# Kernel tuning notes

Measured on AMD Instinct MI355X. Metric: run time of the kernel, lower is better.

## Reference

```python
import jax, jax.numpy as jnp
import numpy as np
from itertools import permutations

M = 10          # number of masked tokens (logits.size(0) when whole_word=False)
VOCAB = 50257   # n_class


def setup_inputs() -> dict:
    key = jax.random.key(0)
    k1, k2 = jax.random.split(key)
    logits = jax.random.normal(k1, (M, VOCAB), dtype=jnp.float32)
    target = jax.random.randint(k2, (M,), 0, VOCAB, dtype=jnp.int64).astype(jnp.int32)
    # All M! permutations, enumerated exactly as itertools.permutations (lexicographic),
    # matching the torch module's iteration order (ties broken by first strict improvement).
    perms = jnp.asarray(np.array(list(permutations(range(M))), dtype=np.int32))
    return {"logits": logits, "target": target, "perms": perms}


def reference(logits, target, perms):
    # prob[i, v] = softmax over classes
    prob = jax.nn.softmax(logits, axis=-1)                      # [M, V]
    # S[i, j] = prob[i, target[j]]  (score of assigning slot j's target to position i)
    S = prob[:, target]                                         # [M, M]
    # score(p) = sum_i prob[i, target[p[i]]] = sum_i S[i, p[i]]
    rows = jnp.arange(S.shape[0], dtype=jnp.int32)[None, :]     # [1, M]
    scores = S[rows, perms].sum(axis=-1)                        # [P]
    # torch loop keeps the FIRST permutation achieving the max (strict > update);
    # jnp.argmax also returns the first occurrence of the max.
    best = jnp.argmax(scores)
    target_best = target[perms[best]]                           # [M]
    # CrossEntropyLoss(reduction='none') == -log_softmax gathered at target
    logp = jax.nn.log_softmax(logits, axis=-1)                  # [M, V]
    loss = -jnp.take_along_axis(logp, target_best[:, None].astype(jnp.int32), axis=1)[:, 0]
    return loss, target_best
```

## Files before the change

kernel.cpp:

```cpp
#include <hip/hip_runtime.h>

#define VOCAB 50257
#define M 10
#define NPERM 3628800
#define CHUNKS 16
#define CH 3144
#define NTHREADS_PERM 30240
#define PERM_BLOCKS 119

#define WS_PSUM 0

__global__ __launch_bounds__(256) void chunkstats_kernel(
    const float* __restrict__ logits, float* __restrict__ ws) {
    const int r = blockIdx.x >> 4;
    const int c = blockIdx.x & 15;
    const size_t rowoff = (size_t)r * VOCAB;
    const float* __restrict__ x = logits + rowoff;
    const int s = c * CH;
    const int e = (s + CH < VOCAB) ? s + CH : VOCAB;
    const int tid = threadIdx.x;
    const int j0 = s + (int)((4u - ((unsigned)rowoff & 3u)) & 3u);
    const int j1 = j0 + ((e - j0) & ~3);
    __shared__ float wred[4];

    float sum = 0.f;
    for (int j = s + tid; j < j0; j += 256) sum += __expf(x[j]);
    for (int j = j0 + 4 * tid; j < j1; j += 1024) {
        const float4 v = *(const float4*)(x + j);
        sum += expf(v.x) + expf(v.y) + expf(v.z) + expf(v.w);
    }
    for (int j = j1 + tid; j < e; j += 256) sum += expf(x[j]);
    #pragma unroll
    for (int off = 32; off; off >>= 1) sum += __shfl_down(sum, off, 64);
    if ((tid & 63) == 0) wred[tid >> 6] = sum;
    __syncthreads();
    if (tid == 0)
        ws[WS_PSUM + blockIdx.x] = wred[0] + wred[1] + wred[2] + wred[3];
}

__global__ __launch_bounds__(256) void perm_kernel(
    const float* __restrict__ logits, const int* __restrict__ target,
    const float* __restrict__ ws, unsigned long long* __restrict__ keys) {
    __shared__ float S[100], rowsum[10];
    __shared__ unsigned long long wk[4];
    const int tid = threadIdx.x;

    if (tid < 160) {
        float c = ws[WS_PSUM + tid];
        #pragma unroll
        for (int off = 8; off; off >>= 1) c += __shfl_xor(c, off, 16);
        if ((tid & 15) == 0) rowsum[tid >> 4] = c;
    }
    __syncthreads();
    if (tid < 100) {
        const int i = tid / 10, k = tid % 10;
        S[tid] = expf(logits[(size_t)i * VOCAB + target[k]]) / rowsum[i];
    }
    __syncthreads();

    const unsigned int t = blockIdx.x * 256u + tid;
    unsigned long long key = 0ull;
    if (t < NTHREADS_PERM) {
        const unsigned int base = t * 120u;
        unsigned int p = base;
        unsigned long long avail = 0x9876543210ull;
        float prefix = 0.f;
        const unsigned int fact5[5] = {362880u, 40320u, 5040u, 720u, 120u};
        #pragma unroll
        for (int pos = 0; pos < 5; ++pos) {
            const unsigned int f = fact5[pos];
            const unsigned int d = p / f;
            p -= d * f;
            const unsigned int sh = d * 4u;
            const unsigned int sym = (unsigned int)(avail >> sh) & 0xFu;
            avail = (avail & ((1ull << sh) - 1ull)) | ((avail >> (sh + 4u)) << sh);
            prefix += S[pos * 10 + sym];
        }
        float s5v[5], s6v[5], s7v[5], s8v[5], s9v[5];
        #pragma unroll
        for (int j = 0; j < 5; ++j) {
            const int q = (int)((avail >> (4 * j)) & 0xFull);
            s5v[j] = S[50 + q]; s6v[j] = S[60 + q]; s7v[j] = S[70 + q];
            s8v[j] = S[80 + q]; s9v[j] = S[90 + q];
        }
        float best = -1.f; unsigned int bl = 0; unsigned int l = 0;
        #pragma unroll
        for (int a = 0; a < 5; ++a) {
            const float pa = prefix + s5v[a];
            #pragma unroll
            for (int b = 0; b < 5; ++b) {
                if (b == a) continue;
                const float pb = pa + s6v[b];
                #pragma unroll
                for (int c = 0; c < 5; ++c) {
                    if (c == a || c == b) continue;
                    const float pc = pb + s7v[c];
                    #pragma unroll
                    for (int d = 0; d < 5; ++d) {
                        if (d == a || d == b || d == c) continue;
                        const int e = 10 - a - b - c - d;
                        const float sc = (pc + s8v[d]) + s9v[e];
                        if (sc > best) { best = sc; bl = l; }
                        ++l;
                    }
                }
            }
        }
        const unsigned int gidx = base + bl;
        key = ((unsigned long long)__float_as_uint(best) << 32) |
              (unsigned long long)(0xFFFFFFFFu - gidx);
    }
    #pragma unroll
    for (int off = 32; off; off >>= 1) {
        const unsigned long long o = __shfl_down(key, off, 64);
        if (o > key) key = o;
    }
    if ((tid & 63) == 0) wk[tid >> 6] = key;
    __syncthreads();
    if (tid == 0) {
        unsigned long long k = wk[0];
        #pragma unroll
        for (int w = 1; w < 4; ++w) if (wk[w] > k) k = wk[w];
        keys[blockIdx.x] = k;
    }
}

__global__ __launch_bounds__(256) void final_kernel(
    const float* __restrict__ logits, const int* __restrict__ target,
    const float* __restrict__ ws, const unsigned long long* __restrict__ keys,
    float* __restrict__ out) {
    __shared__ float rowsum[10];
    __shared__ unsigned long long wk[4];
    __shared__ int perm[10];
    const int tid = threadIdx.x;

    if (tid < 160) {
        float c = ws[WS_PSUM + tid];
        #pragma unroll
        for (int off = 8; off; off >>= 1) c += __shfl_xor(c, off, 16);
        if ((tid & 15) == 0) rowsum[tid >> 4] = c;
    }

    unsigned long long k = (tid < PERM_BLOCKS) ? keys[tid] : 0ull;
    #pragma unroll
    for (int off = 32; off; off >>= 1) {
        const unsigned long long o = __shfl_down(k, off, 64);
        if (o > k) k = o;
    }
    if ((tid & 63) == 0) wk[tid >> 6] = k;
    __syncthreads();
    if (tid == 0) {
        unsigned long long kk = wk[0];
        #pragma unroll
        for (int w = 1; w < 4; ++w) if (wk[w] > kk) kk = wk[w];
        unsigned int p = 0xFFFFFFFFu - (unsigned int)(kk & 0xFFFFFFFFull);
        unsigned long long avail = 0x9876543210ull;
        const unsigned int fact[9] = {362880u, 40320u, 5040u, 720u, 120u, 24u, 6u, 2u, 1u};
        #pragma unroll
        for (int pos = 0; pos < 9; ++pos) {
            const unsigned int f = fact[pos];
            const unsigned int d = p / f;
            p -= d * f;
            const unsigned int sh = d * 4u;
            perm[pos] = (int)((avail >> sh) & 0xFull);
            avail = (avail & ((1ull << sh) - 1ull)) | ((avail >> (sh + 4u)) << sh);
        }
        perm[9] = (int)(avail & 0xFull);
    }
    __syncthreads();
    if (tid < 10) {
        const int tb = target[perm[tid]];
        const float logp = logits[(size_t)tid * VOCAB + tb] - logf(rowsum[tid]);
        out[tid]      = -logp;
        out[10 + tid] = (float)tb;
    }
}

extern "C" void kernel_launch(void* const* d_in, const int* in_sizes, int n_in,
                              void* d_out, int out_size, void* d_ws, size_t ws_size,
                              hipStream_t stream) {
    const float* logits = (const float*)d_in[0];
    const int*   target = (const int*)d_in[1];
    float* ws = (float*)d_ws;
    unsigned long long* keys = (unsigned long long*)((char*)d_ws + 4096);
    float* out = (float*)d_out;

    chunkstats_kernel<<<10 * CHUNKS, 256, 0, stream>>>(logits, ws);
    perm_kernel<<<PERM_BLOCKS, 256, 0, stream>>>(logits, target, ws, keys);
    final_kernel<<<1, 256, 0, stream>>>(logits, target, ws, keys, out);
}
```

Measured before the change: 16.54 us.

## Fuse final reduction into perm kernel via atomic max and last-block pattern

Removes the separate final kernel launch. Each perm block now does an atomicMax of its packed key into a global best and increments a counter, and the last block to finish decodes the winning permutation and writes the outputs. The counter and best slot are reset at the start of the stats kernel. Perm blocks grow to 512 threads with half as many blocks, which trades launch overhead for atomics and a fence, and for fewer, larger blocks across the CUs.

```diff
diff --git a/kernel.cpp b/kernel.cpp
--- a/kernel.cpp
+++ b/kernel.cpp
@@ -6,12 +6,17 @@
 #define CHUNKS 16
 #define CH 3144
 #define NTHREADS_PERM 30240
-#define PERM_BLOCKS 119
+#define PERM_BLOCKS 60
 
 #define WS_PSUM 0
 
 __global__ __launch_bounds__(256) void chunkstats_kernel(
-    const float* __restrict__ logits, float* __restrict__ ws) {
+    const float* __restrict__ logits, float* __restrict__ ws,
+    unsigned int* __restrict__ counter, unsigned long long* __restrict__ best) {
+    if (blockIdx.x == 0 && threadIdx.x == 0) {
+        atomicExch(counter, 0u);
+        atomicExch(best, 0ull);
+    }
     const int r = blockIdx.x >> 4;
     const int c = blockIdx.x & 15;
     const size_t rowoff = (size_t)r * VOCAB;
@@ -24,7 +29,7 @@
     __shared__ float wred[4];
 
     float sum = 0.f;
-    for (int j = s + tid; j < j0; j += 256) sum += __expf(x[j]);
+    for (int j = s + tid; j < j0; j += 256) sum += expf(x[j]);
     for (int j = j0 + 4 * tid; j < j1; j += 1024) {
         const float4 v = *(const float4*)(x + j);
         sum += expf(v.x) + expf(v.y) + expf(v.z) + expf(v.w);
@@ -38,11 +43,14 @@
         ws[WS_PSUM + blockIdx.x] = wred[0] + wred[1] + wred[2] + wred[3];
 }
 
-__global__ __launch_bounds__(256) void perm_kernel(
+__global__ __launch_bounds__(512) void perm_final_kernel(
     const float* __restrict__ logits, const int* __restrict__ target,
-    const float* __restrict__ ws, unsigned long long* __restrict__ keys) {
+    const float* __restrict__ ws, unsigned long long* __restrict__ best,
+    unsigned int* __restrict__ counter, float* __restrict__ out) {
     __shared__ float S[100], rowsum[10];
-    __shared__ unsigned long long wk[4];
+    __shared__ unsigned long long wk[8];
+    __shared__ int perm[10];
+    __shared__ int lastFlag;
     const int tid = threadIdx.x;
 
     if (tid < 160) {
@@ -58,7 +66,7 @@
     }
     __syncthreads();
 
-    const unsigned int t = blockIdx.x * 256u + tid;
+    const unsigned int t = blockIdx.x * 512u + tid;
     unsigned long long key = 0ull;
     if (t < NTHREADS_PERM) {
         const unsigned int base = t * 120u;
@@ -83,7 +91,7 @@
             s5v[j] = S[50 + q]; s6v[j] = S[60 + q]; s7v[j] = S[70 + q];
             s8v[j] = S[80 + q]; s9v[j] = S[90 + q];
         }
-        float best = -1.f; unsigned int bl = 0; unsigned int l = 0;
+        float bestsc = -1.f; unsigned int bl = 0; unsigned int l = 0;
         #pragma unroll
         for (int a = 0; a < 5; ++a) {
             const float pa = prefix + s5v[a];
@@ -100,14 +108,14 @@
                         if (d == a || d == b || d == c) continue;
                         const int e = 10 - a - b - c - d;
                         const float sc = (pc + s8v[d]) + s9v[e];
-                        if (sc > best) { best = sc; bl = l; }
+                        if (sc > bestsc) { bestsc = sc; bl = l; }
                         ++l;
                     }
                 }
             }
         }
         const unsigned int gidx = base + bl;
-        key = ((unsigned long long)__float_as_uint(best) << 32) |
+        key = ((unsigned long long)__float_as_uint(bestsc) << 32) |
               (unsigned long long)(0xFFFFFFFFu - gidx);
     }
     #pragma unroll
@@ -120,39 +128,17 @@
     if (tid == 0) {
         unsigned long long k = wk[0];
         #pragma unroll
-        for (int w = 1; w < 4; ++w) if (wk[w] > k) k = wk[w];
-        keys[blockIdx.x] = k;
+        for (int w = 1; w < 8; ++w) if (wk[w] > k) k = wk[w];
+        atomicMax(best, k);
+        __threadfence();
+        const unsigned int prev = atomicAdd(counter, 1u);
+        lastFlag = (prev == PERM_BLOCKS - 1) ? 1 : 0;
     }
-}
+    __syncthreads();
+    if (!lastFlag) return;
 
-__global__ __launch_bounds__(256) void final_kernel(
-    const float* __restrict__ logits, const int* __restrict__ target,
-    const float* __restrict__ ws, const unsigned long long* __restrict__ keys,
-    float* __restrict__ out) {
-    __shared__ float rowsum[10];
-    __shared__ unsigned long long wk[4];
-    __shared__ int perm[10];
-    const int tid = threadIdx.x;
-
-    if (tid < 160) {
-        float c = ws[WS_PSUM + tid];
-        #pragma unroll
-        for (int off = 8; off; off >>= 1) c += __shfl_xor(c, off, 16);
-        if ((tid & 15) == 0) rowsum[tid >> 4] = c;
-    }
-
-    unsigned long long k = (tid < PERM_BLOCKS) ? keys[tid] : 0ull;
-    #pragma unroll
-    for (int off = 32; off; off >>= 1) {
-        const unsigned long long o = __shfl_down(k, off, 64);
-        if (o > k) k = o;
-    }
-    if ((tid & 63) == 0) wk[tid >> 6] = k;
-    __syncthreads();
     if (tid == 0) {
-        unsigned long long kk = wk[0];
-        #pragma unroll
-        for (int w = 1; w < 4; ++w) if (wk[w] > kk) kk = wk[w];
+        const unsigned long long kk = atomicAdd(best, 0ull);
         unsigned int p = 0xFFFFFFFFu - (unsigned int)(kk & 0xFFFFFFFFull);
         unsigned long long avail = 0x9876543210ull;
         const unsigned int fact[9] = {362880u, 40320u, 5040u, 720u, 120u, 24u, 6u, 2u, 1u};
@@ -182,10 +168,11 @@
     const float* logits = (const float*)d_in[0];
     const int*   target = (const int*)d_in[1];
     float* ws = (float*)d_ws;
-    unsigned long long* keys = (unsigned long long*)((char*)d_ws + 4096);
+    unsigned int* counter = (unsigned int*)((char*)d_ws + 2048);
+    unsigned long long* best = (unsigned long long*)((char*)d_ws + 2056);
     float* out = (float*)d_out;
 
-    chunkstats_kernel<<<10 * CHUNKS, 256, 0, stream>>>(logits, ws);
-    perm_kernel<<<PERM_BLOCKS, 256, 0, stream>>>(logits, target, ws, keys);
-    final_kernel<<<1, 256, 0, stream>>>(logits, target, ws, keys, out);
+    chunkstats_kernel<<<10 * CHUNKS, 256, 0, stream>>>(logits, ws, counter, best);
+    perm_final_kernel<<<PERM_BLOCKS, 512, 0, stream>>>(logits, target, ws, best,
+                                                       counter, out);
 }
```

Result: no change. 16.32 us (median of 2 runs) (-1.3%).
